# Kernel tuning notes

Hardware: AMD Instinct MI355X
Metric: run time of the kernel (lower is better)

## Reference

```python
import jax, jax.numpy as jnp
import numpy as np

INPUT_SIZE = 512
HIDDEN_SIZE = 4096
OUTPUT_SIZE = 512
BATCH = 16384

def _xavier_uniform(key, shape):
    fan_out, fan_in = shape
    limit = np.sqrt(6.0 / (fan_in + fan_out)).astype(np.float32)
    return jax.random.uniform(key, shape, jnp.float32, -limit, limit)

def setup_inputs() -> dict:
    key = jax.random.key(0)
    kx, kk, kg = jax.random.split(key, 3)
    x = jax.random.normal(kx, (BATCH, INPUT_SIZE), dtype=jnp.float32)
    kohonen_weights = _xavier_uniform(kk, (HIDDEN_SIZE, INPUT_SIZE))
    grossberg_weights = _xavier_uniform(kg, (OUTPUT_SIZE, HIDDEN_SIZE))
    return {"x": x, "kohonen_weights": kohonen_weights, "grossberg_weights": grossberg_weights}

def reference(x, kohonen_weights, grossberg_weights):
    # cdist (euclidean): sq distances suffice for argmin; sqrt kept for faithfulness
    x_sq = jnp.sum(x * x, axis=1, keepdims=True)                # [B,1]
    w_sq = jnp.sum(kohonen_weights * kohonen_weights, axis=1)   # [H]
    sq = x_sq - 2.0 * (x @ kohonen_weights.T) + w_sq[None, :]   # [B,H]
    distances = jnp.sqrt(jnp.maximum(sq, 0.0))
    winner_indices = jnp.argmin(distances, axis=1)              # [B]
    # one-hot @ grossberg.T == gather rows of grossberg.T
    output = jnp.take(grossberg_weights.T, winner_indices, axis=0)  # [B,O]
    return (output, winner_indices)
```

## Files before the change

### kernel.cpp

```cpp
#include <hip/hip_runtime.h>
#include <cstdint>
#include <cstddef>

#define B_ 16384
#define K_ 512
#define H_ 4096
#define O_ 512

typedef __attribute__((ext_vector_type(4))) float f32x4;
typedef __attribute__((ext_vector_type(8))) short bf16x8;

#define EPS_FLAG 0.125f

__device__ inline unsigned short f32_to_bf16_rne(float f) {
  unsigned u = __float_as_uint(f);
  unsigned r = (u + 0x7fffu + ((u >> 16) & 1u)) >> 16;
  return (unsigned short)r;
}

__device__ float np_pairwise_sumsq512(const float* __restrict__ a) {
  float s[4];
  #pragma unroll
  for (int blk = 0; blk < 4; ++blk) {
    const float* p = a + blk * 128;
    float r[8];
    #pragma unroll
    for (int j = 0; j < 8; ++j) r[j] = __fmul_rn(p[j], p[j]);
    for (int i = 8; i < 128; i += 8) {
      #pragma unroll
      for (int j = 0; j < 8; ++j) r[j] = __fadd_rn(r[j], __fmul_rn(p[i + j], p[i + j]));
    }
    s[blk] = __fadd_rn(__fadd_rn(__fadd_rn(r[0], r[1]), __fadd_rn(r[2], r[3])),
                       __fadd_rn(__fadd_rn(r[4], r[5]), __fadd_rn(r[6], r[7])));
  }
  return __fadd_rn(__fadd_rn(s[0], s[1]), __fadd_rn(s[2], s[3]));
}

__global__ __launch_bounds__(256) void prep_rows_kernel(
    const float* __restrict__ src, unsigned short* __restrict__ hi,
    float* __restrict__ sumsq, int nrows) {
  __shared__ float buf[8 * 512];
  const int r0 = blockIdx.x * 8;
  const int tid = (int)threadIdx.x;

  #pragma unroll
  for (int it = 0; it < 4; ++it) {
    int i = tid + it * 256;
    float4 v = ((const float4*)(src + (size_t)r0 * K_))[i];
    ((float4*)buf)[i] = v;
    ushort4 h;
    h.x = f32_to_bf16_rne(v.x);
    h.y = f32_to_bf16_rne(v.y);
    h.z = f32_to_bf16_rne(v.z);
    h.w = f32_to_bf16_rne(v.w);
    ((ushort4*)(hi + (size_t)r0 * K_))[i] = h;
  }
  __syncthreads();

  const int row = tid >> 5, l = tid & 31, blk = l >> 3, j = l & 7;
  const float* p = buf + row * 512 + blk * 128;
  float r = __fmul_rn(p[j], p[j]);
  #pragma unroll
  for (int i = 8; i < 128; i += 8) r = __fadd_rn(r, __fmul_rn(p[i + j], p[i + j]));
  r = __fadd_rn(r, __shfl_xor(r, 1));
  r = __fadd_rn(r, __shfl_xor(r, 2));
  r = __fadd_rn(r, __shfl_xor(r, 4));
  r = __fadd_rn(r, __shfl_xor(r, 8));
  r = __fadd_rn(r, __shfl_xor(r, 16));
  if (l == 0 && r0 + row < nrows) sumsq[r0 + row] = r;
}

__global__ void rowsumsq_kernel(const float* __restrict__ src, float* __restrict__ dst,
                                int nrows) {
  int r = blockIdx.x * blockDim.x + threadIdx.x;
  if (r < nrows) dst[r] = np_pairwise_sumsq512(src + (size_t)r * K_);
}

__global__ void transposeG_kernel(const float* __restrict__ G, float* __restrict__ GT) {
  __shared__ float t[32][33];
  int h0 = blockIdx.x * 32, o0 = blockIdx.y * 32;
  for (int i = threadIdx.y; i < 32; i += 8)
    t[i][threadIdx.x] = G[(size_t)(o0 + i) * H_ + h0 + threadIdx.x];
  __syncthreads();
  for (int i = threadIdx.y; i < 32; i += 8)
    GT[(size_t)(h0 + i) * O_ + o0 + threadIdx.x] = t[threadIdx.x][i];
}

__device__ inline void stage_tile64(char* lds_base, const unsigned short* __restrict__ src,
                                    int row0, int kt, int wid, int lane) {
  #pragma unroll
  for (int j = 0; j < 4; ++j) {
    int chunk = wid + j * 4;
    int u = chunk * 64 + lane;
    int row = u >> 3, slot = u & 7;
    int slot_src = slot ^ (row & 7);
    const char* g = (const char*)src + (size_t)(row0 + row) * (K_ * 2) + kt * 128 + slot_src * 16;
    char* l = lds_base + chunk * 1024;
    __builtin_amdgcn_global_load_lds((const __attribute__((address_space(1))) void*)g,
                                     (__attribute__((address_space(3))) void*)l,
                                     16, 0, 0);
  }
}

__global__ __launch_bounds__(256) void phase1_mfma_kernel(
    const unsigned short* __restrict__ xhi, const unsigned short* __restrict__ whi,
    const float* __restrict__ wsq, const float* __restrict__ xsq,
    float* __restrict__ gmin16 ,
    unsigned short* __restrict__ mk16 ) {
  __shared__ __align__(16) char smem[65536];
  const int tid = (int)threadIdx.x;
  const int wid = tid >> 6, lane = tid & 63;
  const int wr = wid >> 1, wc = wid & 1;
  const int cb = blockIdx.y;
  const int row0 = blockIdx.x * 128, col0 = cb * 128;

  f32x4 acc[4][4];
  #pragma unroll
  for (int i = 0; i < 4; ++i)
    #pragma unroll
    for (int j = 0; j < 4; ++j) acc[i][j] = (f32x4){0.f, 0.f, 0.f, 0.f};

  const int arow = wr * 64 + (lane & 15);
  const int brow = wc * 64 + (lane & 15);
  const int r7 = lane & 7, sg = lane >> 4;
  const int offK0 = ((sg ^ r7) & 7) * 16;
  const int offK1 = (((4 + sg) ^ r7) & 7) * 16;

  stage_tile64(smem, xhi, row0, 0, wid, lane);
  stage_tile64(smem + 16384, whi, col0, 0, wid, lane);
  __syncthreads();

  int buf = 0;
  for (int kt = 0; kt < 8; ++kt) {
    if (kt < 7) {
      stage_tile64(smem + (buf ^ 1) * 32768, xhi, row0, kt + 1, wid, lane);
      stage_tile64(smem + (buf ^ 1) * 32768 + 16384, whi, col0, kt + 1, wid, lane);
    }
    const char* A = smem + buf * 32768;
    const char* Bm = smem + buf * 32768 + 16384;
    #pragma unroll
    for (int ks = 0; ks < 2; ++ks) {
      const int offK = ks ? offK1 : offK0;
      bf16x8 ah[4];
      #pragma unroll
      for (int mf = 0; mf < 4; ++mf)
        ah[mf] = *(const bf16x8*)(A + (arow + mf * 16) * 128 + offK);
      #pragma unroll
      for (int nf = 0; nf < 4; ++nf) {
        bf16x8 bh = *(const bf16x8*)(Bm + (brow + nf * 16) * 128 + offK);
        #pragma unroll
        for (int mf = 0; mf < 4; ++mf)
          acc[mf][nf] = __builtin_amdgcn_mfma_f32_16x16x32_bf16(ah[mf], bh, acc[mf][nf], 0, 0, 0);
      }
    }
    __syncthreads();
    buf ^= 1;
  }

  float* T = (float*)smem + wid * (16 * 65);
  float* EpiF = (float*)(smem + 16640);
  unsigned short* EpiM = (unsigned short*)(smem + 21248);

  const float xq = xsq[row0 + wr * 64 + lane];
  const int c = lane & 15;

  #pragma unroll
  for (int nf = 0; nf < 4; ++nf) {
    float wq = wsq[col0 + wc * 64 + nf * 16 + c];
    #pragma unroll
    for (int mf = 0; mf < 4; ++mf)
      #pragma unroll
      for (int r = 0; r < 4; ++r)
        T[c * 65 + (mf * 16 + sg * 4 + r)] = wq - 2.0f * acc[mf][nf][r];
    asm volatile("s_waitcnt lgkmcnt(0)" ::: "memory");
    __builtin_amdgcn_sched_barrier(0);
    float v[16];
    #pragma unroll
    for (int c2 = 0; c2 < 16; ++c2) v[c2] = T[c2 * 65 + lane];
    float mn = v[0];
    #pragma unroll
    for (int c2 = 1; c2 < 16; ++c2) mn = fminf(mn, v[c2]);
    unsigned msk = 0;
    #pragma unroll
    for (int c2 = 0; c2 < 16; ++c2)
      if ((v[c2] <= mn + EPS_FLAG) || (v[c2] + xq <= EPS_FLAG)) msk |= 1u << c2;
    EpiF[(wr * 64 + lane) * 9 + wc * 4 + nf] = mn;
    EpiM[(wr * 64 + lane) * 8 + wc * 4 + nf] = (unsigned short)msk;
  }
  __syncthreads();

  {
    int row = tid >> 1, half = tid & 1;
    float4 vf;
    vf.x = EpiF[row * 9 + half * 4 + 0];
    vf.y = EpiF[row * 9 + half * 4 + 1];
    vf.z = EpiF[row * 9 + half * 4 + 2];
    vf.w = EpiF[row * 9 + half * 4 + 3];
    *(float4*)&gmin16[(size_t)(row0 + row) * 256 + cb * 8 + half * 4] = vf;
    if (tid < 128) {
      uint4 vm = *(const uint4*)&EpiM[tid * 8];
      *(uint4*)&mk16[(size_t)(row0 + tid) * 256 + cb * 8] = vm;
    }
  }
}

#define P2_ROWS 16
#define P2_CAP 2048

__global__ __launch_bounds__(256) void phase2_block_kernel(
    const float* __restrict__ gm ,
    const unsigned short* __restrict__ mk ,
    const float* __restrict__ x, const float* __restrict__ W,
    const float* __restrict__ xsq, const float* __restrict__ wsq,
    const float* __restrict__ GT, float* __restrict__ out) {
  __shared__ float xls[P2_ROWS * 516];
  __shared__ unsigned short clist[P2_CAP];
  __shared__ unsigned long long bestkey[P2_ROWS];
  __shared__ int ncand;
  const int tid = (int)threadIdx.x;
  const int r = tid >> 4, t16 = tid & 15;
  const int b0 = blockIdx.x * P2_ROWS;
  const int b = b0 + r;

  if (tid < P2_ROWS) bestkey[tid] = 0xFFFFFFFFFFFFFFFFULL;
  if (tid == 0) ncand = 0;

  #pragma unroll
  for (int it = 0; it < 8; ++it) {
    int idx = tid + it * 256;
    int xr = idx >> 7, xw = idx & 127;
    float4 v = ((const float4*)(x + (size_t)(b0 + xr) * K_))[xw];
    *(float4*)&xls[xr * 516 + xw * 4] = v;
  }

  float gv[16];
  #pragma unroll
  for (int j = 0; j < 4; ++j) {
    float4 v = *(const float4*)(gm + (size_t)b * 256 + t16 * 16 + j * 4);
    gv[j * 4 + 0] = v.x;
    gv[j * 4 + 1] = v.y;
    gv[j * 4 + 2] = v.z;
    gv[j * 4 + 3] = v.w;
  }
  unsigned short mv[16];
  #pragma unroll
  for (int j = 0; j < 2; ++j) {
    uint4 u = *(const uint4*)(mk + (size_t)b * 256 + t16 * 16 + j * 8);
    mv[j * 8 + 0] = (unsigned short)(u.x & 0xFFFF);
    mv[j * 8 + 1] = (unsigned short)(u.x >> 16);
    mv[j * 8 + 2] = (unsigned short)(u.y & 0xFFFF);
    mv[j * 8 + 3] = (unsigned short)(u.y >> 16);
    mv[j * 8 + 4] = (unsigned short)(u.z & 0xFFFF);
    mv[j * 8 + 5] = (unsigned short)(u.z >> 16);
    mv[j * 8 + 6] = (unsigned short)(u.w & 0xFFFF);
    mv[j * 8 + 7] = (unsigned short)(u.w >> 16);
  }

  float mn = gv[0];
  #pragma unroll
  for (int j = 1; j < 16; ++j) mn = fminf(mn, gv[j]);
  #pragma unroll
  for (int off = 1; off < 16; off <<= 1) mn = fminf(mn, __shfl_xor(mn, off, 16));
  const float xq = xsq[b];
  const float thr = mn + EPS_FLAG;
  __syncthreads();

  #pragma unroll
  for (int j = 0; j < 16; ++j) {
    float v = gv[j];
    if ((v <= thr) || (v + xq <= EPS_FLAG)) {
      int g = t16 * 16 + j;
      unsigned mbits = mv[j];
      while (mbits) {
        int bit = __ffs(mbits) - 1;
        mbits &= mbits - 1;
        int slot = atomicAdd(&ncand, 1);
        if (slot < P2_CAP)
          clist[slot] = (unsigned short)((r << 12) | (g * 16 + bit));
      }
    }
  }
  __syncthreads();

  int total = ncand;
  if (total <= P2_CAP) {
    for (int i = tid; i < total; i += 256) {
      unsigned e = clist[i];
      int rr = (int)(e >> 12);
      int col = (int)(e & 0xFFF);
      const float* xr = xls + rr * 516;
      const float4* wrow = (const float4*)(W + (size_t)col * K_);
      float acc = 0.0f;
      #pragma unroll 8
      for (int kq = 0; kq < K_ / 4; ++kq) {
        float4 xv = *(const float4*)&xr[kq * 4];
        float4 wv = wrow[kq];
        acc = fmaf(xv.x, wv.x, acc);
        acc = fmaf(xv.y, wv.y, acc);
        acc = fmaf(xv.z, wv.z, acc);
        acc = fmaf(xv.w, wv.w, acc);
      }
      float xqr = xsq[b0 + rr];
      float t2 = xqr - 2.0f * acc;
      float sq = t2 + wsq[col];
      float d = sqrtf(fmaxf(sq, 0.0f));
      unsigned long long key =
          ((unsigned long long)__float_as_uint(d) << 32) | (unsigned)col;
      atomicMin(&bestkey[rr], key);
    }
  } else {
    for (int cc = t16; cc < H_; cc += 16) {
      int g = cc >> 4;
      float gvv = gm[(size_t)b * 256 + g];
      if ((gvv <= thr || gvv + xq <= EPS_FLAG) &&
          ((mk[(size_t)b * 256 + g] >> (cc & 15)) & 1)) {
        const float* xr = xls + r * 516;
        const float4* wrow = (const float4*)(W + (size_t)cc * K_);
        float acc = 0.0f;
        #pragma unroll 8
        for (int kq = 0; kq < K_ / 4; ++kq) {
          float4 xv = *(const float4*)&xr[kq * 4];
          float4 wv = wrow[kq];
          acc = fmaf(xv.x, wv.x, acc);
          acc = fmaf(xv.y, wv.y, acc);
          acc = fmaf(xv.z, wv.z, acc);
          acc = fmaf(xv.w, wv.w, acc);
        }
        float t2 = xq - 2.0f * acc;
        float sq = t2 + wsq[cc];
        float d = sqrtf(fmaxf(sq, 0.0f));
        unsigned long long key =
            ((unsigned long long)__float_as_uint(d) << 32) | (unsigned)cc;
        atomicMin(&bestkey[r], key);
      }
    }
  }
  __syncthreads();

  {
    const unsigned h = (unsigned)(bestkey[r] & 0xFFFFFFFFULL);
    const float4* gsrc = (const float4*)(GT + (size_t)h * O_);
    float4* gdst = (float4*)(out + (size_t)b * O_);
    #pragma unroll
    for (int j = 0; j < 8; ++j) gdst[j * 16 + t16] = gsrc[j * 16 + t16];
    if (t16 == 0) out[(size_t)B_ * O_ + b] = (float)h;
  }
}

#define BM 128
#define BN 128
#define BKK 16

__global__ void init_keys_kernel(unsigned long long* __restrict__ keys) {
  int i = blockIdx.x * blockDim.x + threadIdx.x;
  if (i < B_) keys[i] = 0xFFFFFFFFFFFFFFFFULL;
}

__global__ __launch_bounds__(256) void dist_argmin_kernel(
    const float* __restrict__ x, const float* __restrict__ W,
    const float* __restrict__ xsq, const float* __restrict__ wsq,
    unsigned long long* __restrict__ keys) {
  __shared__ float xs[BKK][BM + 4];
  __shared__ float wsh[BKK][BN + 4];
  const int row0 = blockIdx.x * BM;
  const int col0 = blockIdx.y * BN;
  const int tid = (int)threadIdx.x;
  const int tx = tid & 15, ty = tid >> 4;

  float acc[8][8];
  #pragma unroll
  for (int i = 0; i < 8; ++i)
    #pragma unroll
    for (int j = 0; j < 8; ++j) acc[i][j] = 0.0f;

  for (int kt = 0; kt < K_; kt += BKK) {
    #pragma unroll
    for (int l = 0; l < 2; ++l) {
      int e = tid + l * 256;
      int r = e >> 2, kq = e & 3;
      float4 v = *(const float4*)(x + (size_t)(row0 + r) * K_ + kt + kq * 4);
      xs[kq * 4 + 0][r] = v.x;
      xs[kq * 4 + 1][r] = v.y;
      xs[kq * 4 + 2][r] = v.z;
      xs[kq * 4 + 3][r] = v.w;
      float4 u = *(const float4*)(W + (size_t)(col0 + r) * K_ + kt + kq * 4);
      wsh[kq * 4 + 0][r] = u.x;
      wsh[kq * 4 + 1][r] = u.y;
      wsh[kq * 4 + 2][r] = u.z;
      wsh[kq * 4 + 3][r] = u.w;
    }
    __syncthreads();
    #pragma unroll
    for (int k = 0; k < BKK; ++k) {
      float4 a0 = *(const float4*)&xs[k][ty * 4];
      float4 a1 = *(const float4*)&xs[k][ty * 4 + 64];
      float4 b0 = *(const float4*)&wsh[k][tx * 4];
      float4 b1 = *(const float4*)&wsh[k][tx * 4 + 64];
      float ar[8] = {a0.x, a0.y, a0.z, a0.w, a1.x, a1.y, a1.z, a1.w};
      float br[8] = {b0.x, b0.y, b0.z, b0.w, b1.x, b1.y, b1.z, b1.w};
      #pragma unroll
      for (int i = 0; i < 8; ++i)
        #pragma unroll
        for (int j = 0; j < 8; ++j)
          acc[i][j] = fmaf(ar[i], br[j], acc[i][j]);
    }
    __syncthreads();
  }

  float xv[8], wv[8];
  int rowidx[8], colidx[8];
  #pragma unroll
  for (int i = 0; i < 8; ++i) {
    rowidx[i] = row0 + ty * 4 + (i & 3) + (i >> 2) * 64;
    xv[i] = xsq[rowidx[i]];
  }
  #pragma unroll
  for (int j = 0; j < 8; ++j) {
    colidx[j] = col0 + tx * 4 + (j & 3) + (j >> 2) * 64;
    wv[j] = wsq[colidx[j]];
  }
  #pragma unroll
  for (int i = 0; i < 8; ++i) {
    unsigned long long best = 0xFFFFFFFFFFFFFFFFULL;
    #pragma unroll
    for (int j = 0; j < 8; ++j) {
      float t2 = xv[i] - 2.0f * acc[i][j];
      float sq = t2 + wv[j];
      float d = sqrtf(fmaxf(sq, 0.0f));
      unsigned long long key =
          ((unsigned long long)__float_as_uint(d) << 32) | (unsigned)colidx[j];
      best = key < best ? key : best;
    }
    #pragma unroll
    for (int off = 1; off < 16; off <<= 1) {
      unsigned long long o = __shfl_xor(best, off, 16);
      best = o < best ? o : best;
    }
    if (tx == 0) atomicMin(&keys[rowidx[i]], best);
  }
}

__global__ void finalize_kernel(const unsigned long long* __restrict__ keys,
                                const float* __restrict__ GT,
                                const float* __restrict__ G,
                                float* __restrict__ out, int useGT) {
  int b = blockIdx.x;
  unsigned h = (unsigned)(keys[b] & 0xFFFFFFFFULL);
  if (threadIdx.x == 0) out[(size_t)B_ * O_ + b] = (float)h;
  if (useGT) {
    const float4* src = (const float4*)(GT + (size_t)h * O_);
    float4* dst = (float4*)(out + (size_t)b * O_);
    for (int i = threadIdx.x; i < O_ / 4; i += blockDim.x) dst[i] = src[i];
  } else {
    for (int o = threadIdx.x; o < O_; o += blockDim.x)
      out[(size_t)b * O_ + o] = G[(size_t)o * H_ + h];
  }
}

extern "C" void kernel_launch(void* const* d_in, const int* in_sizes, int n_in,
                              void* d_out, int out_size, void* d_ws, size_t ws_size,
                              hipStream_t stream) {
  const float* x = (const float*)d_in[0];
  const float* W = (const float*)d_in[1];
  const float* G = (const float*)d_in[2];
  float* out = (float*)d_out;
  char* ws = (char*)d_ws;

  size_t o_xsq  = 0;
  size_t o_wsq  = o_xsq + 65536;
  size_t o_xhi  = o_wsq + 16384;
  size_t o_whi  = o_xhi + (size_t)B_ * K_ * 2;
  size_t o_gm   = o_whi + (size_t)H_ * K_ * 2;
  size_t o_mk   = o_gm + (size_t)B_ * 256 * 4;
  size_t o_gt   = o_mk + (size_t)B_ * 256 * 2;
  size_t need   = o_gt + (size_t)H_ * O_ * 4;

  if (ws_size >= need) {
    float* xsq = (float*)(ws + o_xsq);
    float* wsq = (float*)(ws + o_wsq);
    unsigned short* xhi = (unsigned short*)(ws + o_xhi);
    unsigned short* whi = (unsigned short*)(ws + o_whi);
    float* gm = (float*)(ws + o_gm);
    unsigned short* mk = (unsigned short*)(ws + o_mk);
    float* GT = (float*)(ws + o_gt);

    hipLaunchKernelGGL(prep_rows_kernel, dim3(B_ / 8), dim3(256), 0, stream,
                       x, xhi, xsq, B_);
    hipLaunchKernelGGL(prep_rows_kernel, dim3(H_ / 8), dim3(256), 0, stream,
                       W, whi, wsq, H_);
    hipLaunchKernelGGL(transposeG_kernel, dim3(H_ / 32, O_ / 32), dim3(32, 8), 0, stream,
                       G, GT);
    hipLaunchKernelGGL(phase1_mfma_kernel, dim3(B_ / 128, H_ / 128), dim3(256), 0, stream,
                       xhi, whi, wsq, xsq, gm, mk);
    hipLaunchKernelGGL(phase2_block_kernel, dim3(B_ / P2_ROWS), dim3(256), 0, stream,
                       gm, mk, x, W, xsq, wsq, GT, out);
    return;
  }

  unsigned long long* keys = (unsigned long long*)ws;
  float* xsq = (float*)(ws + 131072);
  float* wsq = (float*)(ws + 131072 + 65536);
  float* GT = (float*)(ws + 131072 + 65536 + 16384);
  size_t base = 131072 + 65536 + 16384;
  int useGT = ws_size >= base + (size_t)H_ * O_ * 4 ? 1 : 0;

  hipLaunchKernelGGL(init_keys_kernel, dim3(B_ / 256), dim3(256), 0, stream, keys);
  hipLaunchKernelGGL(rowsumsq_kernel, dim3(B_ / 256), dim3(256), 0, stream, x, xsq, B_);
  hipLaunchKernelGGL(rowsumsq_kernel, dim3(H_ / 256), dim3(256), 0, stream, W, wsq, H_);
  if (useGT)
    hipLaunchKernelGGL(transposeG_kernel, dim3(H_ / 32, O_ / 32), dim3(32, 8), 0, stream,
                       G, GT);
  hipLaunchKernelGGL(dist_argmin_kernel, dim3(B_ / BM, H_ / BN), dim3(256), 0, stream,
                     x, W, xsq, wsq, keys);
  hipLaunchKernelGGL(finalize_kernel, dim3(B_), dim3(128), 0, stream, keys, GT, G, out,
                     useGT);
}
```

Measured before the change: 128.1 us.

## Enlarge phase-1 MFMA tile to 256x256 and fuse prep kernels into one launch

The distance GEMM kernel moves from a 128x128 tile with 256 threads to a 256x256 tile with 512 threads and 128KB of double-buffered LDS. Each wave now computes 128x64 outputs, which roughly halves global/LDS staging traffic per MFMA. The epilogue and the min/mask output layout are adapted to 16 column groups per block. Separately, the x/W bf16 conversion, the sum-of-squares and the G transpose are merged into a single prep kernel to save launches. The risks are lower occupancy, since the larger LDS footprint likely allows only one block per CU, and higher register pressure.

```diff
diff --git a/kernel.cpp b/kernel.cpp
--- a/kernel.cpp
+++ b/kernel.cpp
@@ -36,38 +36,57 @@
   return __fadd_rn(__fadd_rn(s[0], s[1]), __fadd_rn(s[2], s[3]));
 }
 
-__global__ __launch_bounds__(256) void prep_rows_kernel(
-    const float* __restrict__ src, unsigned short* __restrict__ hi,
-    float* __restrict__ sumsq, int nrows) {
-  __shared__ float buf[8 * 512];
-  const int r0 = blockIdx.x * 8;
+__global__ __launch_bounds__(256) void prep_all_kernel(
+    const float* __restrict__ x, const float* __restrict__ W,
+    const float* __restrict__ G,
+    unsigned short* __restrict__ xhi, unsigned short* __restrict__ whi,
+    float* __restrict__ xsq, float* __restrict__ wsq, float* __restrict__ GT) {
+  const int bid = (int)blockIdx.x;
   const int tid = (int)threadIdx.x;
 
-  #pragma unroll
-  for (int it = 0; it < 4; ++it) {
-    int i = tid + it * 256;
-    float4 v = ((const float4*)(src + (size_t)r0 * K_))[i];
-    ((float4*)buf)[i] = v;
-    ushort4 h;
-    h.x = f32_to_bf16_rne(v.x);
-    h.y = f32_to_bf16_rne(v.y);
-    h.z = f32_to_bf16_rne(v.z);
-    h.w = f32_to_bf16_rne(v.w);
-    ((ushort4*)(hi + (size_t)r0 * K_))[i] = h;
-  }
-  __syncthreads();
-
-  const int row = tid >> 5, l = tid & 31, blk = l >> 3, j = l & 7;
-  const float* p = buf + row * 512 + blk * 128;
-  float r = __fmul_rn(p[j], p[j]);
-  #pragma unroll
-  for (int i = 8; i < 128; i += 8) r = __fadd_rn(r, __fmul_rn(p[i + j], p[i + j]));
-  r = __fadd_rn(r, __shfl_xor(r, 1));
-  r = __fadd_rn(r, __shfl_xor(r, 2));
-  r = __fadd_rn(r, __shfl_xor(r, 4));
-  r = __fadd_rn(r, __shfl_xor(r, 8));
-  r = __fadd_rn(r, __shfl_xor(r, 16));
-  if (l == 0 && r0 + row < nrows) sumsq[r0 + row] = r;
+  if (bid < 2560) {
+    const float* src = bid < 2048 ? x : W;
+    unsigned short* hi = bid < 2048 ? xhi : whi;
+    float* sumsq = bid < 2048 ? xsq : wsq;
+    const int r0 = (bid < 2048 ? bid : bid - 2048) * 8;
+
+    __shared__ float buf[8 * 512];
+    #pragma unroll
+    for (int it = 0; it < 4; ++it) {
+      int i = tid + it * 256;
+      float4 v = ((const float4*)(src + (size_t)r0 * K_))[i];
+      ((float4*)buf)[i] = v;
+      ushort4 h;
+      h.x = f32_to_bf16_rne(v.x);
+      h.y = f32_to_bf16_rne(v.y);
+      h.z = f32_to_bf16_rne(v.z);
+      h.w = f32_to_bf16_rne(v.w);
+      ((ushort4*)(hi + (size_t)r0 * K_))[i] = h;
+    }
+    __syncthreads();
+
+    const int row = tid >> 5, l = tid & 31, blk = l >> 3, j = l & 7;
+    const float* p = buf + row * 512 + blk * 128;
+    float r = __fmul_rn(p[j], p[j]);
+    #pragma unroll
+    for (int i = 8; i < 128; i += 8) r = __fadd_rn(r, __fmul_rn(p[i + j], p[i + j]));
+    r = __fadd_rn(r, __shfl_xor(r, 1));
+    r = __fadd_rn(r, __shfl_xor(r, 2));
+    r = __fadd_rn(r, __shfl_xor(r, 4));
+    r = __fadd_rn(r, __shfl_xor(r, 8));
+    r = __fadd_rn(r, __shfl_xor(r, 16));
+    if (l == 0) sumsq[r0 + row] = r;
+  } else {
+    __shared__ float t[32][33];
+    const int bid2 = bid - 2560;
+    const int h0 = (bid2 & 127) * 32, o0 = (bid2 >> 7) * 32;
+    const int tx = tid & 31, ty = tid >> 5;
+    for (int i = ty; i < 32; i += 8)
+      t[i][tx] = G[(size_t)(o0 + i) * H_ + h0 + tx];
+    __syncthreads();
+    for (int i = ty; i < 32; i += 8)
+      GT[(size_t)(h0 + i) * O_ + o0 + tx] = t[tx][i];
+  }
 }
 
 __global__ void rowsumsq_kernel(const float* __restrict__ src, float* __restrict__ dst,
@@ -86,70 +105,68 @@
     GT[(size_t)(h0 + i) * O_ + o0 + threadIdx.x] = t[threadIdx.x][i];
 }
 
-__device__ inline void stage_tile64(char* lds_base, const unsigned short* __restrict__ src,
-                                    int row0, int kt, int wid, int lane) {
+__device__ inline void stage_panel256(char* lds_panel, const unsigned short* __restrict__ src,
+                                      int rowbase, int kt, int tid) {
   #pragma unroll
   for (int j = 0; j < 4; ++j) {
-    int chunk = wid + j * 4;
-    int u = chunk * 64 + lane;
+    int u = j * 512 + tid;
     int row = u >> 3, slot = u & 7;
-    int slot_src = slot ^ (row & 7);
-    const char* g = (const char*)src + (size_t)(row0 + row) * (K_ * 2) + kt * 128 + slot_src * 16;
-    char* l = lds_base + chunk * 1024;
+    const char* g = (const char*)src + (size_t)(rowbase + row) * (K_ * 2) + kt * 128 +
+                    ((slot ^ (row & 7)) * 16);
     __builtin_amdgcn_global_load_lds((const __attribute__((address_space(1))) void*)g,
-                                     (__attribute__((address_space(3))) void*)l,
+                                     (__attribute__((address_space(3))) void*)(lds_panel + u * 16),
                                      16, 0, 0);
   }
 }
 
-__global__ __launch_bounds__(256) void phase1_mfma_kernel(
+__global__ __launch_bounds__(512, 2) void phase1_mfma_kernel(
     const unsigned short* __restrict__ xhi, const unsigned short* __restrict__ whi,
     const float* __restrict__ wsq, const float* __restrict__ xsq,
     float* __restrict__ gmin16 ,
     unsigned short* __restrict__ mk16 ) {
-  __shared__ __align__(16) char smem[65536];
+  __shared__ __align__(16) char smem[131072];
   const int tid = (int)threadIdx.x;
   const int wid = tid >> 6, lane = tid & 63;
-  const int wr = wid >> 1, wc = wid & 1;
+  const int wr = wid >> 2, wc = wid & 3;
   const int cb = blockIdx.y;
-  const int row0 = blockIdx.x * 128, col0 = cb * 128;
-
-  f32x4 acc[4][4];
-  #pragma unroll
-  for (int i = 0; i < 4; ++i)
+  const int row0 = blockIdx.x * 256, col0 = cb * 256;
+
+  f32x4 acc[8][4];
+  #pragma unroll
+  for (int i = 0; i < 8; ++i)
     #pragma unroll
     for (int j = 0; j < 4; ++j) acc[i][j] = (f32x4){0.f, 0.f, 0.f, 0.f};
 
-  const int arow = wr * 64 + (lane & 15);
-  const int brow = wc * 64 + (lane & 15);
-  const int r7 = lane & 7, sg = lane >> 4;
+  const int r16 = lane & 15, r7 = lane & 7, sg = lane >> 4;
   const int offK0 = ((sg ^ r7) & 7) * 16;
   const int offK1 = (((4 + sg) ^ r7) & 7) * 16;
-
-  stage_tile64(smem, xhi, row0, 0, wid, lane);
-  stage_tile64(smem + 16384, whi, col0, 0, wid, lane);
+  const int arowb = wr * 128 + r16;
+  const int browb = wc * 64 + r16;
+
+  stage_panel256(smem, xhi, row0, 0, tid);
+  stage_panel256(smem + 32768, whi, col0, 0, tid);
   __syncthreads();
 
   int buf = 0;
   for (int kt = 0; kt < 8; ++kt) {
     if (kt < 7) {
-      stage_tile64(smem + (buf ^ 1) * 32768, xhi, row0, kt + 1, wid, lane);
-      stage_tile64(smem + (buf ^ 1) * 32768 + 16384, whi, col0, kt + 1, wid, lane);
-    }
-    const char* A = smem + buf * 32768;
-    const char* Bm = smem + buf * 32768 + 16384;
+      stage_panel256(smem + (buf ^ 1) * 65536, xhi, row0, kt + 1, tid);
+      stage_panel256(smem + (buf ^ 1) * 65536 + 32768, whi, col0, kt + 1, tid);
+    }
+    const char* A = smem + buf * 65536;
+    const char* Bm = smem + buf * 65536 + 32768;
     #pragma unroll
     for (int ks = 0; ks < 2; ++ks) {
       const int offK = ks ? offK1 : offK0;
-      bf16x8 ah[4];
-      #pragma unroll
-      for (int mf = 0; mf < 4; ++mf)
-        ah[mf] = *(const bf16x8*)(A + (arow + mf * 16) * 128 + offK);
+      bf16x8 ah[8];
+      #pragma unroll
+      for (int mf = 0; mf < 8; ++mf)
+        ah[mf] = *(const bf16x8*)(A + (arowb + mf * 16) * 128 + offK);
       #pragma unroll
       for (int nf = 0; nf < 4; ++nf) {
-        bf16x8 bh = *(const bf16x8*)(Bm + (brow + nf * 16) * 128 + offK);
+        bf16x8 bh = *(const bf16x8*)(Bm + (browb + nf * 16) * 128 + offK);
         #pragma unroll
-        for (int mf = 0; mf < 4; ++mf)
+        for (int mf = 0; mf < 8; ++mf)
           acc[mf][nf] = __builtin_amdgcn_mfma_f32_16x16x32_bf16(ah[mf], bh, acc[mf][nf], 0, 0, 0);
       }
     }
@@ -157,50 +174,52 @@
     buf ^= 1;
   }
 
-  float* T = (float*)smem + wid * (16 * 65);
-  float* EpiF = (float*)(smem + 16640);
-  unsigned short* EpiM = (unsigned short*)(smem + 21248);
-
-  const float xq = xsq[row0 + wr * 64 + lane];
-  const int c = lane & 15;
+  float* T = (float*)smem + wid * (16 * 129);
+  float* EpiF = (float*)(smem + 66048);
+  unsigned short* EpiM = (unsigned short*)(smem + 82432);
+
+  const float xq0 = xsq[row0 + wr * 128 + lane];
+  const float xq1 = xsq[row0 + wr * 128 + 64 + lane];
+  const int c = r16;
 
   #pragma unroll
   for (int nf = 0; nf < 4; ++nf) {
     float wq = wsq[col0 + wc * 64 + nf * 16 + c];
     #pragma unroll
-    for (int mf = 0; mf < 4; ++mf)
+    for (int mf = 0; mf < 8; ++mf)
       #pragma unroll
       for (int r = 0; r < 4; ++r)
-        T[c * 65 + (mf * 16 + sg * 4 + r)] = wq - 2.0f * acc[mf][nf][r];
+        T[c * 129 + mf * 16 + sg * 4 + r] = wq - 2.0f * acc[mf][nf][r];
     asm volatile("s_waitcnt lgkmcnt(0)" ::: "memory");
     __builtin_amdgcn_sched_barrier(0);
-    float v[16];
-    #pragma unroll
-    for (int c2 = 0; c2 < 16; ++c2) v[c2] = T[c2 * 65 + lane];
-    float mn = v[0];
-    #pragma unroll
-    for (int c2 = 1; c2 < 16; ++c2) mn = fminf(mn, v[c2]);
-    unsigned msk = 0;
-    #pragma unroll
-    for (int c2 = 0; c2 < 16; ++c2)
-      if ((v[c2] <= mn + EPS_FLAG) || (v[c2] + xq <= EPS_FLAG)) msk |= 1u << c2;
-    EpiF[(wr * 64 + lane) * 9 + wc * 4 + nf] = mn;
-    EpiM[(wr * 64 + lane) * 8 + wc * 4 + nf] = (unsigned short)msk;
+    #pragma unroll
+    for (int half = 0; half < 2; ++half) {
+      int lrow = lane + half * 64;
+      float xq = half ? xq1 : xq0;
+      float v[16];
+      #pragma unroll
+      for (int c2 = 0; c2 < 16; ++c2) v[c2] = T[c2 * 129 + lrow];
+      float mn = v[0];
+      #pragma unroll
+      for (int c2 = 1; c2 < 16; ++c2) mn = fminf(mn, v[c2]);
+      unsigned msk = 0;
+      #pragma unroll
+      for (int c2 = 0; c2 < 16; ++c2)
+        if ((v[c2] <= mn + EPS_FLAG) || (v[c2] + xq <= EPS_FLAG)) msk |= 1u << c2;
+      EpiF[(wr * 128 + lrow) * 16 + wc * 4 + nf] = mn;
+      EpiM[(wr * 128 + lrow) * 16 + wc * 4 + nf] = (unsigned short)msk;
+    }
   }
   __syncthreads();
 
   {
-    int row = tid >> 1, half = tid & 1;
-    float4 vf;
-    vf.x = EpiF[row * 9 + half * 4 + 0];
-    vf.y = EpiF[row * 9 + half * 4 + 1];
-    vf.z = EpiF[row * 9 + half * 4 + 2];
-    vf.w = EpiF[row * 9 + half * 4 + 3];
-    *(float4*)&gmin16[(size_t)(row0 + row) * 256 + cb * 8 + half * 4] = vf;
-    if (tid < 128) {
-      uint4 vm = *(const uint4*)&EpiM[tid * 8];
-      *(uint4*)&mk16[(size_t)(row0 + tid) * 256 + cb * 8] = vm;
-    }
+    int row = tid >> 1, hf = tid & 1;
+    const float* fr = EpiF + row * 16 + hf * 8;
+    size_t gbase = (size_t)(row0 + row) * 256 + cb * 16 + hf * 8;
+    *(float4*)&gmin16[gbase] = *(const float4*)fr;
+    *(float4*)&gmin16[gbase + 4] = *(const float4*)(fr + 4);
+    uint4 mv = *(const uint4*)(EpiM + row * 16 + hf * 8);
+    *(uint4*)&mk16[gbase] = mv;
   }
 }
 
@@ -484,13 +503,9 @@
     unsigned short* mk = (unsigned short*)(ws + o_mk);
     float* GT = (float*)(ws + o_gt);
 
-    hipLaunchKernelGGL(prep_rows_kernel, dim3(B_ / 8), dim3(256), 0, stream,
-                       x, xhi, xsq, B_);
-    hipLaunchKernelGGL(prep_rows_kernel, dim3(H_ / 8), dim3(256), 0, stream,
-                       W, whi, wsq, H_);
-    hipLaunchKernelGGL(transposeG_kernel, dim3(H_ / 32, O_ / 32), dim3(32, 8), 0, stream,
-                       G, GT);
-    hipLaunchKernelGGL(phase1_mfma_kernel, dim3(B_ / 128, H_ / 128), dim3(256), 0, stream,
+    hipLaunchKernelGGL(prep_all_kernel, dim3(2048 + 512 + 2048), dim3(256), 0, stream,
+                       x, W, G, xhi, whi, xsq, wsq, GT);
+    hipLaunchKernelGGL(phase1_mfma_kernel, dim3(B_ / 256, H_ / 256), dim3(512), 0, stream,
                        xhi, whi, wsq, xsq, gm, mk);
     hipLaunchKernelGGL(phase2_block_kernel, dim3(B_ / P2_ROWS), dim3(256), 0, stream,
                        gm, mk, x, W, xsq, wsq, GT, out);
```

Result: faster. 119.4 us, median of 2 (-6.8%).
